# Kernel optimization log

Measured on AMD Instinct MI355X. Metric: run time of the kernel, lower is better.

The kernel has to match this reference:

```python
import jax, jax.numpy as jnp
import numpy as np

N = 1024
OBS_RADIUS = 0.5


def setup_inputs() -> dict:
    key = jax.random.key(0)
    ks = jax.random.split(key, 16)
    def w(k, shape, fan_in):
        return jax.random.normal(k, shape, dtype=jnp.float32) / np.sqrt(fan_in).astype(np.float32)
    return {
        "s": jax.random.normal(ks[0], (N, 4), dtype=jnp.float32),
        "g": jax.random.normal(ks[1], (N, 2), dtype=jnp.float32),
        "conv1_w": w(ks[2], (64, 5), 5),   "conv1_b": jnp.zeros((64,), jnp.float32),
        "conv2_w": w(ks[3], (128, 64), 64), "conv2_b": jnp.zeros((128,), jnp.float32),
        "fc1_w": w(ks[4], (64, 132), 132), "fc1_b": jnp.zeros((64,), jnp.float32),
        "fc2_w": w(ks[5], (128, 64), 64),  "fc2_b": jnp.zeros((128,), jnp.float32),
        "fc3_w": w(ks[6], (64, 128), 128), "fc3_b": jnp.zeros((64,), jnp.float32),
        "fc4_w": w(ks[7], (4, 64), 64),    "fc4_b": jnp.zeros((4,), jnp.float32),
    }


def reference(s, g, conv1_w, conv1_b, conv2_w, conv2_b,
              fc1_w, fc1_b, fc2_w, fc2_b, fc3_w, fc3_b, fc4_w, fc4_b):
    n = s.shape[0]
    # pairwise agent diff + identity channel: [n, n, 5]
    pd = s[:, None, :] - s[None, :, :]
    x = jnp.concatenate([pd, jnp.eye(n, dtype=s.dtype)[:, :, None]], axis=2)
    # neighbor mask from positional distance: [n, n, 1]
    dist = jnp.linalg.norm(x[:, :, :2], axis=2, keepdims=True)
    mask = (dist < OBS_RADIUS).astype(s.dtype)
    # 1x1-conv edge MLPs (pointwise over the j dim): [n, n, 64] -> [n, n, 128]
    h = jax.nn.relu(jnp.einsum('ijc,oc->ijo', x, conv1_w) + conv1_b)
    h = jax.nn.relu(jnp.einsum('ijc,oc->ijo', h, conv2_w) + conv2_b)
    # masked max-pool over neighbors j: [n, 128]
    pooled = jnp.max(h * mask, axis=1)
    sg = s[:, :2] - g
    feat = jnp.concatenate([pooled, sg, s[:, 2:]], axis=1)  # [n, 132]
    z = jax.nn.relu(feat @ fc1_w.T + fc1_b)
    z = jax.nn.relu(z @ fc2_w.T + fc2_b)
    z = jax.nn.relu(z @ fc3_w.T + fc3_b)
    k = 2.0 * jax.nn.sigmoid(z @ fc4_w.T + fc4_b) - 1.0  # [n, 4]
    k1, k2, k3, k4 = k[:, 0:1], k[:, 1:2], k[:, 2:3], k[:, 3:4]
    zr = jnp.zeros_like(k1)
    gain_x = -jnp.concatenate([k1, zr, k2, zr], axis=1)
    gain_y = -jnp.concatenate([zr, k3, zr, k4], axis=1)
    state = jnp.concatenate([sg, s[:, 2:]], axis=1)  # [n, 4]
    a_x = jnp.sum(state * gain_x, axis=1, keepdims=True)
    a_y = jnp.sum(state * gain_y, axis=1, keepdims=True)
    return jnp.concatenate([a_x, a_y], axis=1)  # [n, 2]
```

## Files before the change

### kernel.cpp

```cpp
#include <hip/hip_runtime.h>

typedef unsigned int u32;
typedef unsigned short u16;
typedef _Float16 f16;
typedef f16 f16x8 __attribute__((ext_vector_type(8)));
typedef float f32x4 __attribute__((ext_vector_type(4)));

#define NTH 256
#define SH1 72

__global__ __launch_bounds__(NTH) void NetworkAction_86131274154571_kernel(
    const float* __restrict__ s,    const float* __restrict__ g,
    const float* __restrict__ w1g,  const float* __restrict__ b1g,
    const float* __restrict__ w2g,  const float* __restrict__ b2g,
    const float* __restrict__ fc1w, const float* __restrict__ fc1b,
    const float* __restrict__ fc2w, const float* __restrict__ fc2b,
    const float* __restrict__ fc3w, const float* __restrict__ fc3b,
    const float* __restrict__ fc4w, const float* __restrict__ fc4b,
    float2* __restrict__ out)
{
    __shared__ float4 acts[1024];
    __shared__ int    actj[1024];
    __shared__ f16    h1buf[16][SH1];
    __shared__ float  w1s[320];
    __shared__ float  b1s[64];
    __shared__ float  feat[132];
    __shared__ float  z1[64];
    __shared__ float  z2[128];
    __shared__ float  z3[64];
    __shared__ float  kk[4];
    __shared__ int    cnt;

    const int tid  = threadIdx.x;
    const int lane = tid & 63;
    const int wave = tid >> 6;
    const int i    = blockIdx.x;

    if (tid == 0) cnt = 0;
    for (int q = tid; q < 320; q += NTH) w1s[q] = w1g[q];
    if (tid < 64) b1s[tid] = b1g[tid];
    __syncthreads();

    const float4 si = ((const float4*)s)[i];

    #pragma unroll
    for (int p = 0; p < 4; ++p) {
        const int j = p * NTH + tid;
        float4 sj = ((const float4*)s)[j];
        float dx = si.x - sj.x, dy = si.y - sj.y;
        if (dx * dx + dy * dy < 0.25f) {
            int slot = atomicAdd(&cnt, 1);
            acts[slot] = sj;
            actj[slot] = j;
        }
    }
    __syncthreads();
    const int n_act = cnt;

    const int n_base = wave * 32;
    const int ncol   = lane & 15;
    const int kq     = lane >> 4;
    f16x8 bfrag[2][2];
    float b2r[2];
    #pragma unroll
    for (int tile = 0; tile < 2; ++tile) {
        const int n = n_base + tile * 16 + ncol;
        b2r[tile] = b2g[n];
        #pragma unroll
        for (int t = 0; t < 2; ++t) {
            const float* wp = w2g + n * 64 + t * 32 + kq * 8;
            float4 lo = ((const float4*)wp)[0];
            float4 hi = ((const float4*)wp)[1];
            f16x8 b;
            b[0] = (f16)lo.x; b[1] = (f16)lo.y; b[2] = (f16)lo.z; b[3] = (f16)lo.w;
            b[4] = (f16)hi.x; b[5] = (f16)hi.y; b[6] = (f16)hi.z; b[7] = (f16)hi.w;
            bfrag[tile][t] = b;
        }
    }

    float mtile[2] = {0.0f, 0.0f};

    for (int gbase = 0; gbase < n_act; gbase += 16) {
        #pragma unroll
        for (int it = 0; it < 2; ++it) {
            const int idx = it * NTH + tid;
            const int p = idx >> 5, c2 = idx & 31;
            if (gbase + p < n_act) {
                const float4 sj = acts[gbase + p];
                const float x0 = si.x - sj.x, x1 = si.y - sj.y;
                const float x2 = si.z - sj.z, x3 = si.w - sj.w;
                const float x4 = (actj[gbase + p] == i) ? 1.0f : 0.0f;
                const int c = c2 * 2;
                const float* wa = &w1s[c * 5];
                float ha = b1s[c];
                ha = fmaf(wa[0], x0, ha); ha = fmaf(wa[1], x1, ha);
                ha = fmaf(wa[2], x2, ha); ha = fmaf(wa[3], x3, ha);
                ha = fmaf(wa[4], x4, ha);
                const float* wb = &w1s[c * 5 + 5];
                float hb = b1s[c + 1];
                hb = fmaf(wb[0], x0, hb); hb = fmaf(wb[1], x1, hb);
                hb = fmaf(wb[2], x2, hb); hb = fmaf(wb[3], x3, hb);
                hb = fmaf(wb[4], x4, hb);
                f16 fa = (f16)fmaxf(ha, 0.0f);
                f16 fb = (f16)fmaxf(hb, 0.0f);
                u32 pk = (u32)__builtin_bit_cast(u16, fa) |
                         ((u32)__builtin_bit_cast(u16, fb) << 16);
                *(u32*)&h1buf[p][c2 * 2] = pk;
            }
        }
        __syncthreads();

        f16x8 afr[2];
        #pragma unroll
        for (int t = 0; t < 2; ++t)
            afr[t] = *(const f16x8*)&h1buf[ncol][t * 32 + kq * 8];

        #pragma unroll
        for (int tile = 0; tile < 2; ++tile) {
            f32x4 acc = {0.0f, 0.0f, 0.0f, 0.0f};
            acc = __builtin_amdgcn_mfma_f32_16x16x32_f16(afr[0], bfrag[tile][0], acc, 0, 0, 0);
            acc = __builtin_amdgcn_mfma_f32_16x16x32_f16(afr[1], bfrag[tile][1], acc, 0, 0, 0);
            #pragma unroll
            for (int r = 0; r < 4; ++r) {
                const bool valid = (gbase + kq * 4 + r) < n_act;
                const float v = acc[r] + b2r[tile];
                mtile[tile] = valid ? fmaxf(mtile[tile], v) : mtile[tile];
            }
        }
        __syncthreads();
    }

    #pragma unroll
    for (int tile = 0; tile < 2; ++tile) {
        float m = mtile[tile];
        m = fmaxf(m, __shfl_xor(m, 16));
        m = fmaxf(m, __shfl_xor(m, 32));
        if (lane < 16) feat[n_base + tile * 16 + lane] = m;
    }
    if (tid == 0) {
        float2 gi = ((const float2*)g)[i];
        feat[128] = si.x - gi.x;
        feat[129] = si.y - gi.y;
        feat[130] = si.z;
        feat[131] = si.w;
    }
    __syncthreads();

    if (tid < 64) {
        float acc = fc1b[tid];
        const float4* wv = (const float4*)(fc1w + tid * 132);
        #pragma unroll
        for (int q = 0; q < 33; ++q) {
            float4 u = wv[q];
            int k = q * 4;
            acc = fmaf(u.x, feat[k+0], acc);
            acc = fmaf(u.y, feat[k+1], acc);
            acc = fmaf(u.z, feat[k+2], acc);
            acc = fmaf(u.w, feat[k+3], acc);
        }
        z1[tid] = fmaxf(acc, 0.0f);
    }
    __syncthreads();

    if (tid < 128) {
        float acc = fc2b[tid];
        const float4* wv = (const float4*)(fc2w + tid * 64);
        #pragma unroll
        for (int q = 0; q < 16; ++q) {
            float4 u = wv[q];
            int k = q * 4;
            acc = fmaf(u.x, z1[k+0], acc);
            acc = fmaf(u.y, z1[k+1], acc);
            acc = fmaf(u.z, z1[k+2], acc);
            acc = fmaf(u.w, z1[k+3], acc);
        }
        z2[tid] = fmaxf(acc, 0.0f);
    }
    __syncthreads();

    if (tid < 64) {
        float acc = fc3b[tid];
        const float4* wv = (const float4*)(fc3w + tid * 128);
        #pragma unroll
        for (int q = 0; q < 32; ++q) {
            float4 u = wv[q];
            int k = q * 4;
            acc = fmaf(u.x, z2[k+0], acc);
            acc = fmaf(u.y, z2[k+1], acc);
            acc = fmaf(u.z, z2[k+2], acc);
            acc = fmaf(u.w, z2[k+3], acc);
        }
        z3[tid] = fmaxf(acc, 0.0f);
    }
    __syncthreads();

    if (tid < 4) {
        float acc = fc4b[tid];
        const float4* wv = (const float4*)(fc4w + tid * 64);
        #pragma unroll
        for (int q = 0; q < 16; ++q) {
            float4 u = wv[q];
            int k = q * 4;
            acc = fmaf(u.x, z3[k+0], acc);
            acc = fmaf(u.y, z3[k+1], acc);
            acc = fmaf(u.z, z3[k+2], acc);
            acc = fmaf(u.w, z3[k+3], acc);
        }
        kk[tid] = 2.0f / (1.0f + expf(-acc)) - 1.0f;
    }
    __syncthreads();

    if (tid == 0) {
        float ax = -(kk[0] * feat[128] + kk[1] * feat[130]);
        float ay = -(kk[2] * feat[129] + kk[3] * feat[131]);
        out[i] = make_float2(ax, ay);
    }
}

extern "C" void kernel_launch(void* const* d_in, const int* in_sizes, int n_in,
                              void* d_out, int out_size, void* d_ws, size_t ws_size,
                              hipStream_t stream) {
    const float* s    = (const float*)d_in[0];
    const float* g    = (const float*)d_in[1];
    const float* c1w  = (const float*)d_in[2];
    const float* c1b  = (const float*)d_in[3];
    const float* c2w  = (const float*)d_in[4];
    const float* c2b  = (const float*)d_in[5];
    const float* fc1w = (const float*)d_in[6];
    const float* fc1b = (const float*)d_in[7];
    const float* fc2w = (const float*)d_in[8];
    const float* fc2b = (const float*)d_in[9];
    const float* fc3w = (const float*)d_in[10];
    const float* fc3b = (const float*)d_in[11];
    const float* fc4w = (const float*)d_in[12];
    const float* fc4b = (const float*)d_in[13];

    float2* out = (float2*)d_out;

    NetworkAction_86131274154571_kernel<<<1024, NTH, 0, stream>>>(
        s, g, c1w, c1b, c2w, c2b, fc1w, fc1b, fc2w, fc2b,
        fc3w, fc3b, fc4w, fc4b, out);
}
```

Measured before the change: 98.10 us.

## Shrink blocks to a single wave with ballot compaction and register-held weights

Each block now runs as one 64-thread wave instead of four waves. Neighbor compaction uses a ballot/popcount prefix instead of a shared-memory atomic counter. The conv1 weights live in per-lane registers, and each lane computes one hidden channel. The wave runs all 8 MFMA output tiles itself, and the FC layers use split accumulators plus a shuffle-reduced fc4. The goal is to cut the cost of block-wide barriers, atomics and idle threads in the serial MLP tail. In exchange, each block has less parallelism and each lane holds more registers (8x2 B fragments).

```diff
diff --git a/kernel.cpp b/kernel.cpp
--- a/kernel.cpp
+++ b/kernel.cpp
@@ -6,10 +6,9 @@
 typedef f16 f16x8 __attribute__((ext_vector_type(8)));
 typedef float f32x4 __attribute__((ext_vector_type(4)));
 
-#define NTH 256
 #define SH1 72
 
-__global__ __launch_bounds__(NTH) void NetworkAction_86131274154571_kernel(
+__global__ __launch_bounds__(64) void NetworkAction_86131274154571_kernel(
     const float* __restrict__ s,    const float* __restrict__ g,
     const float* __restrict__ w1g,  const float* __restrict__ b1g,
     const float* __restrict__ w2g,  const float* __restrict__ b2g,
@@ -19,52 +18,31 @@
     const float* __restrict__ fc4w, const float* __restrict__ fc4b,
     float2* __restrict__ out)
 {
-    __shared__ float4 acts[1024];
-    __shared__ int    actj[1024];
+    __shared__ float4 actx[1024];
+    __shared__ float  actf[1024];
     __shared__ f16    h1buf[16][SH1];
-    __shared__ float  w1s[320];
-    __shared__ float  b1s[64];
     __shared__ float  feat[132];
     __shared__ float  z1[64];
     __shared__ float  z2[128];
     __shared__ float  z3[64];
     __shared__ float  kk[4];
-    __shared__ int    cnt;
-
-    const int tid  = threadIdx.x;
-    const int lane = tid & 63;
-    const int wave = tid >> 6;
+
+    const int lane = threadIdx.x;
     const int i    = blockIdx.x;
-
-    if (tid == 0) cnt = 0;
-    for (int q = tid; q < 320; q += NTH) w1s[q] = w1g[q];
-    if (tid < 64) b1s[tid] = b1g[tid];
-    __syncthreads();
+    const int ncol = lane & 15;
+    const int kq   = lane >> 4;
 
     const float4 si = ((const float4*)s)[i];
 
-    #pragma unroll
-    for (int p = 0; p < 4; ++p) {
-        const int j = p * NTH + tid;
-        float4 sj = ((const float4*)s)[j];
-        float dx = si.x - sj.x, dy = si.y - sj.y;
-        if (dx * dx + dy * dy < 0.25f) {
-            int slot = atomicAdd(&cnt, 1);
-            acts[slot] = sj;
-            actj[slot] = j;
-        }
-    }
-    __syncthreads();
-    const int n_act = cnt;
-
-    const int n_base = wave * 32;
-    const int ncol   = lane & 15;
-    const int kq     = lane >> 4;
-    f16x8 bfrag[2][2];
-    float b2r[2];
-    #pragma unroll
-    for (int tile = 0; tile < 2; ++tile) {
-        const int n = n_base + tile * 16 + ncol;
+    const float* wp1 = w1g + lane * 5;
+    const float w10 = wp1[0], w11 = wp1[1], w12 = wp1[2], w13 = wp1[3], w14 = wp1[4];
+    const float b1r = b1g[lane];
+
+    f16x8 bfrag[8][2];
+    float b2r[8];
+    #pragma unroll
+    for (int tile = 0; tile < 8; ++tile) {
+        const int n = tile * 16 + ncol;
         b2r[tile] = b2g[n];
         #pragma unroll
         for (int t = 0; t < 2; ++t) {
@@ -78,34 +56,39 @@
         }
     }
 
-    float mtile[2] = {0.0f, 0.0f};
+    int cnt = 0;
+    #pragma unroll
+    for (int it = 0; it < 16; ++it) {
+        const int j = it * 64 + lane;
+        float4 sj = ((const float4*)s)[j];
+        float dx = si.x - sj.x, dy = si.y - sj.y;
+        bool act = (dx * dx + dy * dy) < 0.25f;
+        unsigned long long m = __ballot(act);
+        if (act) {
+            int pos = cnt + (int)__popcll(m & ((1ull << lane) - 1ull));
+            actx[pos] = make_float4(dx, dy, si.z - sj.z, si.w - sj.w);
+            actf[pos] = (j == i) ? 1.0f : 0.0f;
+        }
+        cnt += (int)__popcll(m);
+    }
+    const int n_act = cnt;
+    __syncthreads();
+
+    float mt[8];
+    #pragma unroll
+    for (int t = 0; t < 8; ++t) mt[t] = 0.0f;
 
     for (int gbase = 0; gbase < n_act; gbase += 16) {
         #pragma unroll
-        for (int it = 0; it < 2; ++it) {
-            const int idx = it * NTH + tid;
-            const int p = idx >> 5, c2 = idx & 31;
+        for (int p = 0; p < 16; ++p) {
             if (gbase + p < n_act) {
-                const float4 sj = acts[gbase + p];
-                const float x0 = si.x - sj.x, x1 = si.y - sj.y;
-                const float x2 = si.z - sj.z, x3 = si.w - sj.w;
-                const float x4 = (actj[gbase + p] == i) ? 1.0f : 0.0f;
-                const int c = c2 * 2;
-                const float* wa = &w1s[c * 5];
-                float ha = b1s[c];
-                ha = fmaf(wa[0], x0, ha); ha = fmaf(wa[1], x1, ha);
-                ha = fmaf(wa[2], x2, ha); ha = fmaf(wa[3], x3, ha);
-                ha = fmaf(wa[4], x4, ha);
-                const float* wb = &w1s[c * 5 + 5];
-                float hb = b1s[c + 1];
-                hb = fmaf(wb[0], x0, hb); hb = fmaf(wb[1], x1, hb);
-                hb = fmaf(wb[2], x2, hb); hb = fmaf(wb[3], x3, hb);
-                hb = fmaf(wb[4], x4, hb);
-                f16 fa = (f16)fmaxf(ha, 0.0f);
-                f16 fb = (f16)fmaxf(hb, 0.0f);
-                u32 pk = (u32)__builtin_bit_cast(u16, fa) |
-                         ((u32)__builtin_bit_cast(u16, fb) << 16);
-                *(u32*)&h1buf[p][c2 * 2] = pk;
+                const float4 x  = actx[gbase + p];
+                const float  x4 = actf[gbase + p];
+                float h = b1r;
+                h = fmaf(w10, x.x, h); h = fmaf(w11, x.y, h);
+                h = fmaf(w12, x.z, h); h = fmaf(w13, x.w, h);
+                h = fmaf(w14, x4,  h);
+                h1buf[p][lane] = (f16)fmaxf(h, 0.0f);
             }
         }
         __syncthreads();
@@ -116,7 +99,7 @@
             afr[t] = *(const f16x8*)&h1buf[ncol][t * 32 + kq * 8];
 
         #pragma unroll
-        for (int tile = 0; tile < 2; ++tile) {
+        for (int tile = 0; tile < 8; ++tile) {
             f32x4 acc = {0.0f, 0.0f, 0.0f, 0.0f};
             acc = __builtin_amdgcn_mfma_f32_16x16x32_f16(afr[0], bfrag[tile][0], acc, 0, 0, 0);
             acc = __builtin_amdgcn_mfma_f32_16x16x32_f16(afr[1], bfrag[tile][1], acc, 0, 0, 0);
@@ -124,20 +107,20 @@
             for (int r = 0; r < 4; ++r) {
                 const bool valid = (gbase + kq * 4 + r) < n_act;
                 const float v = acc[r] + b2r[tile];
-                mtile[tile] = valid ? fmaxf(mtile[tile], v) : mtile[tile];
+                mt[tile] = valid ? fmaxf(mt[tile], v) : mt[tile];
             }
         }
         __syncthreads();
     }
 
     #pragma unroll
-    for (int tile = 0; tile < 2; ++tile) {
-        float m = mtile[tile];
+    for (int tile = 0; tile < 8; ++tile) {
+        float m = mt[tile];
         m = fmaxf(m, __shfl_xor(m, 16));
         m = fmaxf(m, __shfl_xor(m, 32));
-        if (lane < 16) feat[n_base + tile * 16 + lane] = m;
-    }
-    if (tid == 0) {
+        if (lane < 16) feat[tile * 16 + lane] = m;
+    }
+    if (lane == 0) {
         float2 gi = ((const float2*)g)[i];
         feat[128] = si.x - gi.x;
         feat[129] = si.y - gi.y;
@@ -146,71 +129,84 @@
     }
     __syncthreads();
 
-    if (tid < 64) {
-        float acc = fc1b[tid];
-        const float4* wv = (const float4*)(fc1w + tid * 132);
+    {
+        float a0 = fc1b[lane], a1 = 0.f, a2 = 0.f, a3 = 0.f;
+        const float4* wv = (const float4*)(fc1w + lane * 132);
         #pragma unroll
         for (int q = 0; q < 33; ++q) {
             float4 u = wv[q];
-            int k = q * 4;
-            acc = fmaf(u.x, feat[k+0], acc);
-            acc = fmaf(u.y, feat[k+1], acc);
-            acc = fmaf(u.z, feat[k+2], acc);
-            acc = fmaf(u.w, feat[k+3], acc);
-        }
-        z1[tid] = fmaxf(acc, 0.0f);
-    }
-    __syncthreads();
-
-    if (tid < 128) {
-        float acc = fc2b[tid];
-        const float4* wv = (const float4*)(fc2w + tid * 64);
+            const int k = q * 4;
+            float* a = (q & 3) == 0 ? &a0 : (q & 3) == 1 ? &a1 : (q & 3) == 2 ? &a2 : &a3;
+            *a = fmaf(u.x, feat[k + 0], *a);
+            *a = fmaf(u.y, feat[k + 1], *a);
+            *a = fmaf(u.z, feat[k + 2], *a);
+            *a = fmaf(u.w, feat[k + 3], *a);
+        }
+        z1[lane] = fmaxf((a0 + a1) + (a2 + a3), 0.0f);
+    }
+    __syncthreads();
+
+    {
+        float aA0 = fc2b[lane],      aA1 = 0.f;
+        float aB0 = fc2b[lane + 64], aB1 = 0.f;
+        const float4* wvA = (const float4*)(fc2w + lane * 64);
+        const float4* wvB = (const float4*)(fc2w + (lane + 64) * 64);
         #pragma unroll
         for (int q = 0; q < 16; ++q) {
-            float4 u = wv[q];
-            int k = q * 4;
-            acc = fmaf(u.x, z1[k+0], acc);
-            acc = fmaf(u.y, z1[k+1], acc);
-            acc = fmaf(u.z, z1[k+2], acc);
-            acc = fmaf(u.w, z1[k+3], acc);
-        }
-        z2[tid] = fmaxf(acc, 0.0f);
-    }
-    __syncthreads();
-
-    if (tid < 64) {
-        float acc = fc3b[tid];
-        const float4* wv = (const float4*)(fc3w + tid * 128);
+            float4 uA = wvA[q];
+            float4 uB = wvB[q];
+            const int k = q * 4;
+            const float f0 = z1[k + 0], f1 = z1[k + 1], f2 = z1[k + 2], f3 = z1[k + 3];
+            if (q & 1) {
+                aA1 = fmaf(uA.x, f0, aA1); aA1 = fmaf(uA.y, f1, aA1);
+                aA1 = fmaf(uA.z, f2, aA1); aA1 = fmaf(uA.w, f3, aA1);
+                aB1 = fmaf(uB.x, f0, aB1); aB1 = fmaf(uB.y, f1, aB1);
+                aB1 = fmaf(uB.z, f2, aB1); aB1 = fmaf(uB.w, f3, aB1);
+            } else {
+                aA0 = fmaf(uA.x, f0, aA0); aA0 = fmaf(uA.y, f1, aA0);
+                aA0 = fmaf(uA.z, f2, aA0); aA0 = fmaf(uA.w, f3, aA0);
+                aB0 = fmaf(uB.x, f0, aB0); aB0 = fmaf(uB.y, f1, aB0);
+                aB0 = fmaf(uB.z, f2, aB0); aB0 = fmaf(uB.w, f3, aB0);
+            }
+        }
+        z2[lane]      = fmaxf(aA0 + aA1, 0.0f);
+        z2[lane + 64] = fmaxf(aB0 + aB1, 0.0f);
+    }
+    __syncthreads();
+
+    {
+        float a0 = fc3b[lane], a1 = 0.f, a2 = 0.f, a3 = 0.f;
+        const float4* wv = (const float4*)(fc3w + lane * 128);
         #pragma unroll
         for (int q = 0; q < 32; ++q) {
             float4 u = wv[q];
-            int k = q * 4;
-            acc = fmaf(u.x, z2[k+0], acc);
-            acc = fmaf(u.y, z2[k+1], acc);
-            acc = fmaf(u.z, z2[k+2], acc);
-            acc = fmaf(u.w, z2[k+3], acc);
-        }
-        z3[tid] = fmaxf(acc, 0.0f);
-    }
-    __syncthreads();
-
-    if (tid < 4) {
-        float acc = fc4b[tid];
-        const float4* wv = (const float4*)(fc4w + tid * 64);
-        #pragma unroll
-        for (int q = 0; q < 16; ++q) {
-            float4 u = wv[q];
-            int k = q * 4;
-            acc = fmaf(u.x, z3[k+0], acc);
-            acc = fmaf(u.y, z3[k+1], acc);
-            acc = fmaf(u.z, z3[k+2], acc);
-            acc = fmaf(u.w, z3[k+3], acc);
-        }
-        kk[tid] = 2.0f / (1.0f + expf(-acc)) - 1.0f;
-    }
-    __syncthreads();
-
-    if (tid == 0) {
+            const int k = q * 4;
+            float* a = (q & 3) == 0 ? &a0 : (q & 3) == 1 ? &a1 : (q & 3) == 2 ? &a2 : &a3;
+            *a = fmaf(u.x, z2[k + 0], *a);
+            *a = fmaf(u.y, z2[k + 1], *a);
+            *a = fmaf(u.z, z2[k + 2], *a);
+            *a = fmaf(u.w, z2[k + 3], *a);
+        }
+        z3[lane] = fmaxf((a0 + a1) + (a2 + a3), 0.0f);
+    }
+    __syncthreads();
+
+    {
+        const int q  = lane >> 4;
+        const int ks = lane & 15;
+        float4 u = ((const float4*)(fc4w + q * 64))[ks];
+        float part = u.x * z3[ks * 4 + 0] + u.y * z3[ks * 4 + 1]
+                   + u.z * z3[ks * 4 + 2] + u.w * z3[ks * 4 + 3];
+        part += __shfl_xor(part, 1);
+        part += __shfl_xor(part, 2);
+        part += __shfl_xor(part, 4);
+        part += __shfl_xor(part, 8);
+        if (ks == 0)
+            kk[q] = 2.0f / (1.0f + expf(-(part + fc4b[q]))) - 1.0f;
+    }
+    __syncthreads();
+
+    if (lane == 0) {
         float ax = -(kk[0] * feat[128] + kk[1] * feat[130]);
         float ay = -(kk[2] * feat[129] + kk[3] * feat[131]);
         out[i] = make_float2(ax, ay);
@@ -237,7 +233,7 @@
 
     float2* out = (float2*)d_out;
 
-    NetworkAction_86131274154571_kernel<<<1024, NTH, 0, stream>>>(
+    NetworkAction_86131274154571_kernel<<<1024, 64, 0, stream>>>(
         s, g, c1w, c1b, c2w, c2b, fc1w, fc1b, fc2w, fc2b,
         fc3w, fc3b, fc4w, fc4b, out);
 }
```

Measured after the change: 105.6 us. 7.7% more time.
